# Optimization experiments

Hardware: AMD Instinct MI355X
Metric: run time of the kernel (lower is better)

## Reference

```python
import jax, jax.numpy as jnp
import numpy as np

B, S, F, D = 4, 1024, 8, 512
H = 8
DK = D // H
DF = 2048
ECLIPSE_BOOST = 2.0
LN_EPS = 1e-5


def _layer_norm(x, g, b):
    m = jnp.mean(x, axis=-1, keepdims=True)
    v = jnp.mean(jnp.square(x - m), axis=-1, keepdims=True)
    return (x - m) * jax.lax.rsqrt(v + LN_EPS) * g + b


def setup_inputs() -> dict:
    key = jax.random.key(0)
    ks = jax.random.split(key, 16)
    def lin_w(k, out_d, in_d):
        return jax.random.normal(k, (out_d, in_d), jnp.float32) * (1.0 / np.sqrt(in_d))
    return {
        "x": jax.random.normal(ks[0], (B, S, F, D), jnp.float32),
        "eclipse_mask": jax.random.bernoulli(ks[1], 0.3, (B, S)),
        "wq": lin_w(ks[2], D, D), "bq": jnp.zeros((D,), jnp.float32),
        "wk": lin_w(ks[3], D, D), "bk": jnp.zeros((D,), jnp.float32),
        "wv": lin_w(ks[4], D, D), "bv": jnp.zeros((D,), jnp.float32),
        "wo": lin_w(ks[5], D, D), "bo": jnp.zeros((D,), jnp.float32),
        "w1": lin_w(ks[6], DF, D), "b1": jnp.zeros((DF,), jnp.float32),
        "w2": lin_w(ks[7], D, DF), "b2": jnp.zeros((D,), jnp.float32),
        "g1": jnp.ones((D,), jnp.float32), "be1": jnp.zeros((D,), jnp.float32),
        "g2": jnp.ones((D,), jnp.float32), "be2": jnp.zeros((D,), jnp.float32),
    }


def reference(x, eclipse_mask, wq, bq, wk, bk, wv, bv, wo, bo, w1, b1, w2, b2, g1, be1, g2, be2):
    BF = B * F
    scale = 1.0 / np.sqrt(DK)
    # NOTE: the torch module does x.view(B*F, S, D) on a [B,S,F,D] tensor —
    # a raw memory reshape (NOT a transpose). Replicate exactly.
    xr = x.reshape(BF, S, D)  # [BF, S, D]
    # eclipse_mask [B,S] -> expand over features -> [BF, S] (rows b*F+f share mask[b])
    em = jnp.broadcast_to(eclipse_mask[:, None, :], (B, F, S)).reshape(BF, S)

    def proj(w, b):
        return (xr @ w.T + b).reshape(BF, S, H, DK).transpose(0, 2, 1, 3)  # [BF,H,S,DK]

    Q, K, V = proj(wq, bq), proj(wk, bk), proj(wv, bv)
    scores = jnp.einsum("bhqd,bhkd->bhqk", Q, K) * scale  # [BF,H,S,S]
    boost = jnp.where(em, ECLIPSE_BOOST, 1.0)[:, None, None, :]  # over key positions
    scores = scores * boost
    attn = jax.nn.softmax(scores, axis=-1)
    ctx = jnp.einsum("bhqk,bhkd->bhqd", attn, V)  # [BF,H,S,DK]
    ctx = ctx.transpose(0, 2, 1, 3).reshape(BF, S, D)
    attn_out = (ctx @ wo.T + bo).reshape(B, S, F, D)  # raw reshape back, matches torch

    h = _layer_norm(x + attn_out, g1, be1)
    ff = jax.nn.gelu(h @ w1.T + b1, approximate=False) @ w2.T + b2
    return _layer_norm(h + ff, g2, be2)
```

## Files before the change

kernel.cpp:

```cpp
#include <hip/hip_runtime.h>
#include <math.h>

typedef _Float16 half8 __attribute__((ext_vector_type(8)));
typedef float f32x4 __attribute__((ext_vector_type(4)));
typedef unsigned int u32;

#define AS1 __attribute__((address_space(1)))
#define AS3 __attribute__((address_space(3)))

__device__ __forceinline__ void g2lds16(const void* g, void* l) {
    __builtin_amdgcn_global_load_lds((const AS1 u32*)g, (AS3 u32*)l, 16, 0, 0);
}

__global__ __launch_bounds__(256)
void cvt_all(const float* __restrict__ x, const float* __restrict__ wq,
             const float* __restrict__ wk, const float* __restrict__ wv,
             const float* __restrict__ wo, const float* __restrict__ w1,
             const float* __restrict__ w2, _Float16* __restrict__ xh,
             _Float16* __restrict__ qkvw, _Float16* __restrict__ woh,
             _Float16* __restrict__ w1h, _Float16* __restrict__ w2h)
{
    const int bid = blockIdx.x;
    const float* src; _Float16* dst; int g;
    if (bid < 8192)      { src = x;  dst = xh;            g = bid*256 + threadIdx.x; }
    else if (bid < 8320) { src = wq; dst = qkvw;          g = (bid-8192)*256 + threadIdx.x; }
    else if (bid < 8448) { src = wk; dst = qkvw + 262144; g = (bid-8320)*256 + threadIdx.x; }
    else if (bid < 8576) { src = wv; dst = qkvw + 524288; g = (bid-8448)*256 + threadIdx.x; }
    else if (bid < 8704) { src = wo; dst = woh;           g = (bid-8576)*256 + threadIdx.x; }
    else if (bid < 9216) { src = w1; dst = w1h;           g = (bid-8704)*256 + threadIdx.x; }
    else                 { src = w2; dst = w2h;           g = (bid-9216)*256 + threadIdx.x; }
    const float4* p = (const float4*)src + (size_t)g * 2;
    float4 a = p[0], b = p[1];
    half8 h;
    h[0]=(_Float16)a.x; h[1]=(_Float16)a.y; h[2]=(_Float16)a.z; h[3]=(_Float16)a.w;
    h[4]=(_Float16)b.x; h[5]=(_Float16)b.y; h[6]=(_Float16)b.z; h[7]=(_Float16)b.w;
    *((half8*)dst + g) = h;
}

__global__ __launch_bounds__(256)
void pack_bias(const float* __restrict__ bq, const float* __restrict__ bk,
               const float* __restrict__ bv, float* __restrict__ o)
{
    const int i = blockIdx.x * 256 + threadIdx.x;
    o[i] = i < 512 ? bq[i] : (i < 1024 ? bk[i-512] : bv[i-1024]);
}

template<int MODE>
__global__ __launch_bounds__(256)
void gemm_bt(const _Float16* __restrict__ A, const _Float16* __restrict__ B,
             const float* __restrict__ bias, const float* __restrict__ resf,
             const _Float16* __restrict__ resh, void* __restrict__ Cout,
             int M, int N, int K)
{
    __shared__ __align__(16) _Float16 As[128 * 32];
    __shared__ __align__(16) _Float16 Bs[128 * 32];
    const int tid = threadIdx.x;
    const int lane = tid & 63;
    const int w = tid >> 6;
    const int wm = w >> 1, wn = w & 1;
    const int m0 = blockIdx.y * 128, n0 = blockIdx.x * 128;
    const int lrow = lane & 15;
    const int lk = (lane >> 4) * 8;

    f32x4 acc[4][4];
#pragma unroll
    for (int i = 0; i < 4; ++i)
#pragma unroll
        for (int j = 0; j < 4; ++j) acc[i][j] = (f32x4)0.0f;

    for (int k0 = 0; k0 < K; k0 += 32) {
#pragma unroll
        for (int i = 0; i < 2; ++i) {
            int gbase = i * 256 + w * 64;
            int g = gbase + lane;
            g2lds16(A + (size_t)(m0 + (g >> 2)) * K + k0 + (g & 3) * 8,
                    (char*)As + (size_t)gbase * 16);
            g2lds16(B + (size_t)(n0 + (g >> 2)) * K + k0 + (g & 3) * 8,
                    (char*)Bs + (size_t)gbase * 16);
        }
        __syncthreads();
        half8 af[4], bfr[4];
#pragma unroll
        for (int t = 0; t < 4; ++t) {
            af[t]  = *(const half8*)(As + (wm * 64 + t * 16 + lrow) * 32 + lk);
            bfr[t] = *(const half8*)(Bs + (wn * 64 + t * 16 + lrow) * 32 + lk);
        }
#pragma unroll
        for (int mi = 0; mi < 4; ++mi)
#pragma unroll
            for (int ni = 0; ni < 4; ++ni)
                acc[mi][ni] = __builtin_amdgcn_mfma_f32_16x16x32_f16(af[mi], bfr[ni], acc[mi][ni], 0, 0, 0);
        __syncthreads();
    }

    const int rq = (lane >> 4) * 4;
#pragma unroll
    for (int mi = 0; mi < 4; ++mi) {
#pragma unroll
        for (int ni = 0; ni < 4; ++ni) {
            const int col = n0 + wn * 64 + ni * 16 + lrow;
            const float bv = bias[col];
#pragma unroll
            for (int r = 0; r < 4; ++r) {
                const int row = m0 + wm * 64 + mi * 16 + rq + r;
                const size_t idx = (size_t)row * N + col;
                float v = acc[mi][ni][r] + bv;
                if (MODE == 0) {
                    ((_Float16*)Cout)[idx] = (_Float16)v;
                } else if (MODE == 1) {
                    float t2 = -1.5957691216057308f * v * fmaf(v * v, 0.044715f, 1.0f);
                    float e = __expf(t2);
                    ((_Float16*)Cout)[idx] = (_Float16)(v * __builtin_amdgcn_rcpf(1.0f + e));
                } else if (MODE == 2) {
                    ((float*)Cout)[idx] = v + resf[idx];
                } else {
                    ((float*)Cout)[idx] = v + (float)resh[idx];
                }
            }
        }
    }
}

__global__ __launch_bounds__(256)
void attn_fwd(const _Float16* __restrict__ QKV, const int* __restrict__ mask,
              _Float16* __restrict__ ctx)
{
    constexpr int SQ = 72;
    __shared__ __align__(16) _Float16 Ks[64 * SQ];
    __shared__ __align__(16) _Float16 Vts[64 * SQ];
    __shared__ __align__(16) _Float16 Ps[4][32 * SQ];
    __shared__ float scs[1024];

    const int tid = threadIdx.x;
    const int lane = tid & 63;
    const int w = tid >> 6;
    const int bf = blockIdx.y >> 3;
    const int hh = blockIdx.y & 7;
    const int q0 = blockIdx.x * 128;
    const int lrow = lane & 15;
    const int lq = lane >> 4;

    {
        const int* mrow = mask + (bf >> 3) * 1024;
        const int i = tid * 4;
        int4 mm = *(const int4*)(mrow + i);
        scs[i + 0] = mm.x ? 0.25f : 0.125f;
        scs[i + 1] = mm.y ? 0.25f : 0.125f;
        scs[i + 2] = mm.z ? 0.25f : 0.125f;
        scs[i + 3] = mm.w ? 0.25f : 0.125f;
    }

    half8 qf[2][2];
#pragma unroll
    for (int qi = 0; qi < 2; ++qi) {
        const _Float16* qp = QKV + (size_t)(bf * 1024 + q0 + w * 32 + qi * 16 + lrow) * 1536 + hh * 64 + lq * 8;
        qf[qi][0] = *(const half8*)qp;
        qf[qi][1] = *(const half8*)(qp + 32);
    }

    const _Float16* Kbase = QKV + (size_t)bf * 1024 * 1536 + 512 + hh * 64;
    const _Float16* Vbase = Kbase + 512;

    f32x4 acc[2][4];
#pragma unroll
    for (int qi = 0; qi < 2; ++qi)
#pragma unroll
        for (int d = 0; d < 4; ++d) acc[qi][d] = (f32x4)0.0f;
    float lpart[2][4] = {{0.f,0.f,0.f,0.f},{0.f,0.f,0.f,0.f}};
    _Float16* Pw = &Ps[w][0];

    for (int kt = 0; kt < 1024; kt += 64) {
        __syncthreads();
        {
            const int r = tid >> 3, c = (tid & 7) * 8;
            *(uint4*)&Ks[r * SQ + c]        = *(const uint4*)(Kbase + (size_t)(kt + r) * 1536 + c);
            *(uint4*)&Ks[(r + 32) * SQ + c] = *(const uint4*)(Kbase + (size_t)(kt + r + 32) * 1536 + c);
            const int key = lane, dvb = w * 16;
            const _Float16* vp = Vbase + (size_t)(kt + key) * 1536 + dvb;
            half8 v0 = *(const half8*)vp;
            half8 v1 = *(const half8*)(vp + 8);
#pragma unroll
            for (int j = 0; j < 8; ++j) Vts[(dvb + j) * SQ + key] = v0[j];
#pragma unroll
            for (int j = 0; j < 8; ++j) Vts[(dvb + 8 + j) * SQ + key] = v1[j];
        }
        __syncthreads();

#pragma unroll
        for (int nt = 0; nt < 4; ++nt) {
            half8 kf0 = *(const half8*)(Ks + (nt * 16 + lrow) * SQ + lq * 8);
            half8 kf1 = *(const half8*)(Ks + (nt * 16 + lrow) * SQ + 32 + lq * 8);
            const float sc = scs[kt + nt * 16 + lrow];
#pragma unroll
            for (int qi = 0; qi < 2; ++qi) {
                f32x4 s = (f32x4)0.0f;
                s = __builtin_amdgcn_mfma_f32_16x16x32_f16(qf[qi][0], kf0, s, 0, 0, 0);
                s = __builtin_amdgcn_mfma_f32_16x16x32_f16(qf[qi][1], kf1, s, 0, 0, 0);
#pragma unroll
                for (int r = 0; r < 4; ++r) {
                    float p = __expf(fmaf(s[r], sc, -5.0f));
                    lpart[qi][r] += p;
                    Pw[(qi * 16 + lq * 4 + r) * SQ + nt * 16 + lrow] = (_Float16)p;
                }
            }
        }

        half8 pf[2][2];
#pragma unroll
        for (int qi = 0; qi < 2; ++qi) {
            pf[qi][0] = *(const half8*)(Pw + (qi * 16 + lrow) * SQ + lq * 8);
            pf[qi][1] = *(const half8*)(Pw + (qi * 16 + lrow) * SQ + 32 + lq * 8);
        }
#pragma unroll
        for (int d = 0; d < 4; ++d) {
            half8 vf0 = *(const half8*)(Vts + (d * 16 + lrow) * SQ + lq * 8);
            half8 vf1 = *(const half8*)(Vts + (d * 16 + lrow) * SQ + 32 + lq * 8);
#pragma unroll
            for (int qi = 0; qi < 2; ++qi) {
                acc[qi][d] = __builtin_amdgcn_mfma_f32_16x16x32_f16(pf[qi][0], vf0, acc[qi][d], 0, 0, 0);
                acc[qi][d] = __builtin_amdgcn_mfma_f32_16x16x32_f16(pf[qi][1], vf1, acc[qi][d], 0, 0, 0);
            }
        }
    }

#pragma unroll
    for (int qi = 0; qi < 2; ++qi) {
#pragma unroll
        for (int r = 0; r < 4; ++r) {
            float l = lpart[qi][r];
            l += __shfl_xor(l, 1); l += __shfl_xor(l, 2);
            l += __shfl_xor(l, 4); l += __shfl_xor(l, 8);
            const float inv = 1.0f / l;
            const int row = q0 + w * 32 + qi * 16 + lq * 4 + r;
            _Float16* cp = ctx + ((size_t)bf * 1024 + row) * 512 + hh * 64;
#pragma unroll
            for (int d = 0; d < 4; ++d)
                cp[d * 16 + lrow] = (_Float16)(acc[qi][d][r] * inv);
        }
    }
}

template<int OUTH>
__global__ __launch_bounds__(256)
void ln_fused(const float* __restrict__ X, const float* __restrict__ gma,
              const float* __restrict__ bta, float* __restrict__ outF,
              _Float16* __restrict__ outH)
{
    const int row = blockIdx.x * 4 + (threadIdx.x >> 6);
    const int lane = threadIdx.x & 63;
    const float4* xr = (const float4*)(X + (size_t)row * 512);
    float4 a = xr[lane * 2], c = xr[lane * 2 + 1];
    float s  = a.x + a.y + a.z + a.w + c.x + c.y + c.z + c.w;
    float s2 = a.x * a.x + a.y * a.y + a.z * a.z + a.w * a.w
             + c.x * c.x + c.y * c.y + c.z * c.z + c.w * c.w;
#pragma unroll
    for (int m = 1; m < 64; m <<= 1) { s += __shfl_xor(s, m); s2 += __shfl_xor(s2, m); }
    const float mean = s * (1.0f / 512.0f);
    const float inv = rsqrtf(s2 * (1.0f / 512.0f) - mean * mean + 1e-5f);
    const float4* gp = (const float4*)gma;
    const float4* bp = (const float4*)bta;
    float4 g0 = gp[lane * 2], g1 = gp[lane * 2 + 1];
    float4 b0 = bp[lane * 2], b1 = bp[lane * 2 + 1];
    float4 o0, o1;
    o0.x = (a.x - mean) * inv * g0.x + b0.x; o0.y = (a.y - mean) * inv * g0.y + b0.y;
    o0.z = (a.z - mean) * inv * g0.z + b0.z; o0.w = (a.w - mean) * inv * g0.w + b0.w;
    o1.x = (c.x - mean) * inv * g1.x + b1.x; o1.y = (c.y - mean) * inv * g1.y + b1.y;
    o1.z = (c.z - mean) * inv * g1.z + b1.z; o1.w = (c.w - mean) * inv * g1.w + b1.w;
    if (OUTH) {
        half8 hv;
        hv[0] = (_Float16)o0.x; hv[1] = (_Float16)o0.y; hv[2] = (_Float16)o0.z; hv[3] = (_Float16)o0.w;
        hv[4] = (_Float16)o1.x; hv[5] = (_Float16)o1.y; hv[6] = (_Float16)o1.z; hv[7] = (_Float16)o1.w;
        *((half8*)(outH + (size_t)row * 512) + lane) = hv;
    } else {
        float4* op = (float4*)(outF + (size_t)row * 512);
        op[lane * 2] = o0; op[lane * 2 + 1] = o1;
    }
}

extern "C" void kernel_launch(void* const* d_in, const int* in_sizes, int n_in,
                              void* d_out, int out_size, void* d_ws, size_t ws_size,
                              hipStream_t stream)
{
    const float* x   = (const float*)d_in[0];
    const int* mask  = (const int*)d_in[1];
    const float* wq  = (const float*)d_in[2];  const float* bq  = (const float*)d_in[3];
    const float* wk  = (const float*)d_in[4];  const float* bk  = (const float*)d_in[5];
    const float* wv  = (const float*)d_in[6];  const float* bv  = (const float*)d_in[7];
    const float* wo  = (const float*)d_in[8];  const float* bo  = (const float*)d_in[9];
    const float* w1  = (const float*)d_in[10]; const float* b1  = (const float*)d_in[11];
    const float* w2  = (const float*)d_in[12]; const float* b2  = (const float*)d_in[13];
    const float* g1  = (const float*)d_in[14]; const float* be1 = (const float*)d_in[15];
    const float* g2  = (const float*)d_in[16]; const float* be2 = (const float*)d_in[17];
    float* out = (float*)d_out;

    char* ws = (char*)d_ws;
    _Float16* qkvh = (_Float16*)(ws);
    _Float16* ctxh = (_Float16*)(ws + 100663296);
    _Float16* gh   = (_Float16*)(ws);
    _Float16* xh   = (_Float16*)(ws + 134217728);
    float*    res  = (float*)   (ws + 134217728);
    _Float16* hhb  = (_Float16*)(ws + 201326592);
    float*    biasf= (float*)   (ws + 201326592);
    _Float16* qkvw = (_Float16*)(ws + 234881024);
    _Float16* woh  = (_Float16*)(ws + 236453888);
    _Float16* w1h  = (_Float16*)(ws + 236978176);
    _Float16* w2h  = (_Float16*)(ws + 239075328);

    dim3 blk(256);

    cvt_all<<<9728, blk, 0, stream>>>(x, wq, wk, wv, wo, w1, w2, xh, qkvw, woh, w1h, w2h);
    pack_bias<<<6, blk, 0, stream>>>(bq, bk, bv, biasf);

    gemm_bt<0><<<dim3(12, 256), blk, 0, stream>>>(xh, qkvw, biasf, nullptr, nullptr, qkvh, 32768, 1536, 512);

    attn_fwd<<<dim3(8, 256), blk, 0, stream>>>(qkvh, mask, ctxh);

    gemm_bt<2><<<dim3(4, 256), blk, 0, stream>>>(ctxh, woh, bo, x, nullptr, res, 32768, 512, 512);

    ln_fused<1><<<8192, blk, 0, stream>>>(res, g1, be1, nullptr, hhb);

    gemm_bt<1><<<dim3(16, 256), blk, 0, stream>>>(hhb, w1h, b1, nullptr, nullptr, gh, 32768, 2048, 512);

    gemm_bt<3><<<dim3(4, 256), blk, 0, stream>>>(gh, w2h, b2, nullptr, hhb, res, 32768, 512, 2048);

    ln_fused<0><<<8192, blk, 0, stream>>>(res, g2, be2, out, nullptr);
}
```

Measured before the change: 696.5 us.

## Store residual sums in fp16, double K-step in GEMM, read mask directly

The residual-plus-projection outputs feeding both layer norms are now stored as fp16 instead of fp32, which halves that intermediate traffic, and the layer-norm kernel reads half8 inputs. The GEMM now loads two 32-wide K slices per barrier pair, halving the number of syncs per K. Attention drops the shared-memory scale table and reads the mask from global memory inside the inner loop. Rounding the residual sum to fp16 before layer norm adds precision loss.

```diff
diff --git a/kernel.cpp b/kernel.cpp
--- a/kernel.cpp
+++ b/kernel.cpp
@@ -52,8 +52,8 @@
              const _Float16* __restrict__ resh, void* __restrict__ Cout,
              int M, int N, int K)
 {
-    __shared__ __align__(16) _Float16 As[128 * 32];
-    __shared__ __align__(16) _Float16 Bs[128 * 32];
+    __shared__ __align__(16) _Float16 As[2][128 * 32];
+    __shared__ __align__(16) _Float16 Bs[2][128 * 32];
     const int tid = threadIdx.x;
     const int lane = tid & 63;
     const int w = tid >> 6;
@@ -68,28 +68,34 @@
 #pragma unroll
         for (int j = 0; j < 4; ++j) acc[i][j] = (f32x4)0.0f;
 
-    for (int k0 = 0; k0 < K; k0 += 32) {
-#pragma unroll
-        for (int i = 0; i < 2; ++i) {
-            int gbase = i * 256 + w * 64;
-            int g = gbase + lane;
-            g2lds16(A + (size_t)(m0 + (g >> 2)) * K + k0 + (g & 3) * 8,
-                    (char*)As + (size_t)gbase * 16);
-            g2lds16(B + (size_t)(n0 + (g >> 2)) * K + k0 + (g & 3) * 8,
-                    (char*)Bs + (size_t)gbase * 16);
+    for (int k0 = 0; k0 < K; k0 += 64) {
+#pragma unroll
+        for (int p = 0; p < 2; ++p) {
+#pragma unroll
+            for (int i = 0; i < 2; ++i) {
+                int gbase = i * 256 + w * 64;
+                int g = gbase + lane;
+                g2lds16(A + (size_t)(m0 + (g >> 2)) * K + k0 + p * 32 + (g & 3) * 8,
+                        (char*)As[p] + (size_t)gbase * 16);
+                g2lds16(B + (size_t)(n0 + (g >> 2)) * K + k0 + p * 32 + (g & 3) * 8,
+                        (char*)Bs[p] + (size_t)gbase * 16);
+            }
         }
         __syncthreads();
-        half8 af[4], bfr[4];
-#pragma unroll
-        for (int t = 0; t < 4; ++t) {
-            af[t]  = *(const half8*)(As + (wm * 64 + t * 16 + lrow) * 32 + lk);
-            bfr[t] = *(const half8*)(Bs + (wn * 64 + t * 16 + lrow) * 32 + lk);
-        }
-#pragma unroll
-        for (int mi = 0; mi < 4; ++mi)
-#pragma unroll
-            for (int ni = 0; ni < 4; ++ni)
-                acc[mi][ni] = __builtin_amdgcn_mfma_f32_16x16x32_f16(af[mi], bfr[ni], acc[mi][ni], 0, 0, 0);
+#pragma unroll
+        for (int p = 0; p < 2; ++p) {
+            half8 af[4], bfr[4];
+#pragma unroll
+            for (int t = 0; t < 4; ++t) {
+                af[t]  = *(const half8*)(&As[p][0] + (wm * 64 + t * 16 + lrow) * 32 + lk);
+                bfr[t] = *(const half8*)(&Bs[p][0] + (wn * 64 + t * 16 + lrow) * 32 + lk);
+            }
+#pragma unroll
+            for (int mi = 0; mi < 4; ++mi)
+#pragma unroll
+                for (int ni = 0; ni < 4; ++ni)
+                    acc[mi][ni] = __builtin_amdgcn_mfma_f32_16x16x32_f16(af[mi], bfr[ni], acc[mi][ni], 0, 0, 0);
+        }
         __syncthreads();
     }
 
@@ -112,9 +118,9 @@
                     float e = __expf(t2);
                     ((_Float16*)Cout)[idx] = (_Float16)(v * __builtin_amdgcn_rcpf(1.0f + e));
                 } else if (MODE == 2) {
-                    ((float*)Cout)[idx] = v + resf[idx];
+                    ((_Float16*)Cout)[idx] = (_Float16)(v + resf[idx]);
                 } else {
-                    ((float*)Cout)[idx] = v + (float)resh[idx];
+                    ((_Float16*)Cout)[idx] = (_Float16)(v + (float)resh[idx]);
                 }
             }
         }
@@ -129,7 +135,6 @@
     __shared__ __align__(16) _Float16 Ks[64 * SQ];
     __shared__ __align__(16) _Float16 Vts[64 * SQ];
     __shared__ __align__(16) _Float16 Ps[4][32 * SQ];
-    __shared__ float scs[1024];
 
     const int tid = threadIdx.x;
     const int lane = tid & 63;
@@ -140,15 +145,7 @@
     const int lrow = lane & 15;
     const int lq = lane >> 4;
 
-    {
-        const int* mrow = mask + (bf >> 3) * 1024;
-        const int i = tid * 4;
-        int4 mm = *(const int4*)(mrow + i);
-        scs[i + 0] = mm.x ? 0.25f : 0.125f;
-        scs[i + 1] = mm.y ? 0.25f : 0.125f;
-        scs[i + 2] = mm.z ? 0.25f : 0.125f;
-        scs[i + 3] = mm.w ? 0.25f : 0.125f;
-    }
+    const int* mrow = mask + (bf >> 3) * 1024;
 
     half8 qf[2][2];
 #pragma unroll
@@ -190,7 +187,7 @@
         for (int nt = 0; nt < 4; ++nt) {
             half8 kf0 = *(const half8*)(Ks + (nt * 16 + lrow) * SQ + lq * 8);
             half8 kf1 = *(const half8*)(Ks + (nt * 16 + lrow) * SQ + 32 + lq * 8);
-            const float sc = scs[kt + nt * 16 + lrow];
+            const float sc = mrow[kt + nt * 16 + lrow] ? 0.25f : 0.125f;
 #pragma unroll
             for (int qi = 0; qi < 2; ++qi) {
                 f32x4 s = (f32x4)0.0f;
@@ -242,17 +239,19 @@
 
 template<int OUTH>
 __global__ __launch_bounds__(256)
-void ln_fused(const float* __restrict__ X, const float* __restrict__ gma,
+void ln_fused(const _Float16* __restrict__ X, const float* __restrict__ gma,
               const float* __restrict__ bta, float* __restrict__ outF,
               _Float16* __restrict__ outH)
 {
     const int row = blockIdx.x * 4 + (threadIdx.x >> 6);
     const int lane = threadIdx.x & 63;
-    const float4* xr = (const float4*)(X + (size_t)row * 512);
-    float4 a = xr[lane * 2], c = xr[lane * 2 + 1];
-    float s  = a.x + a.y + a.z + a.w + c.x + c.y + c.z + c.w;
-    float s2 = a.x * a.x + a.y * a.y + a.z * a.z + a.w * a.w
-             + c.x * c.x + c.y * c.y + c.z * c.z + c.w * c.w;
+    const half8 hv = *((const half8*)(X + (size_t)row * 512) + lane);
+    float v[8];
+#pragma unroll
+    for (int j = 0; j < 8; ++j) v[j] = (float)hv[j];
+    float s = 0.f, s2 = 0.f;
+#pragma unroll
+    for (int j = 0; j < 8; ++j) { s += v[j]; s2 = fmaf(v[j], v[j], s2); }
 #pragma unroll
     for (int m = 1; m < 64; m <<= 1) { s += __shfl_xor(s, m); s2 += __shfl_xor(s2, m); }
     const float mean = s * (1.0f / 512.0f);
@@ -261,19 +260,20 @@
     const float4* bp = (const float4*)bta;
     float4 g0 = gp[lane * 2], g1 = gp[lane * 2 + 1];
     float4 b0 = bp[lane * 2], b1 = bp[lane * 2 + 1];
-    float4 o0, o1;
-    o0.x = (a.x - mean) * inv * g0.x + b0.x; o0.y = (a.y - mean) * inv * g0.y + b0.y;
-    o0.z = (a.z - mean) * inv * g0.z + b0.z; o0.w = (a.w - mean) * inv * g0.w + b0.w;
-    o1.x = (c.x - mean) * inv * g1.x + b1.x; o1.y = (c.y - mean) * inv * g1.y + b1.y;
-    o1.z = (c.z - mean) * inv * g1.z + b1.z; o1.w = (c.w - mean) * inv * g1.w + b1.w;
+    float o[8];
+    o[0] = (v[0]-mean)*inv*g0.x + b0.x; o[1] = (v[1]-mean)*inv*g0.y + b0.y;
+    o[2] = (v[2]-mean)*inv*g0.z + b0.z; o[3] = (v[3]-mean)*inv*g0.w + b0.w;
+    o[4] = (v[4]-mean)*inv*g1.x + b1.x; o[5] = (v[5]-mean)*inv*g1.y + b1.y;
+    o[6] = (v[6]-mean)*inv*g1.z + b1.z; o[7] = (v[7]-mean)*inv*g1.w + b1.w;
     if (OUTH) {
-        half8 hv;
-        hv[0] = (_Float16)o0.x; hv[1] = (_Float16)o0.y; hv[2] = (_Float16)o0.z; hv[3] = (_Float16)o0.w;
-        hv[4] = (_Float16)o1.x; hv[5] = (_Float16)o1.y; hv[6] = (_Float16)o1.z; hv[7] = (_Float16)o1.w;
-        *((half8*)(outH + (size_t)row * 512) + lane) = hv;
+        half8 ho;
+#pragma unroll
+        for (int j = 0; j < 8; ++j) ho[j] = (_Float16)o[j];
+        *((half8*)(outH + (size_t)row * 512) + lane) = ho;
     } else {
         float4* op = (float4*)(outF + (size_t)row * 512);
-        op[lane * 2] = o0; op[lane * 2 + 1] = o1;
+        op[lane * 2]     = make_float4(o[0], o[1], o[2], o[3]);
+        op[lane * 2 + 1] = make_float4(o[4], o[5], o[6], o[7]);
     }
 }
 
@@ -294,17 +294,17 @@
     float* out = (float*)d_out;
 
     char* ws = (char*)d_ws;
-    _Float16* qkvh = (_Float16*)(ws);
-    _Float16* ctxh = (_Float16*)(ws + 100663296);
-    _Float16* gh   = (_Float16*)(ws);
-    _Float16* xh   = (_Float16*)(ws + 134217728);
-    float*    res  = (float*)   (ws + 134217728);
-    _Float16* hhb  = (_Float16*)(ws + 201326592);
-    float*    biasf= (float*)   (ws + 201326592);
-    _Float16* qkvw = (_Float16*)(ws + 234881024);
-    _Float16* woh  = (_Float16*)(ws + 236453888);
-    _Float16* w1h  = (_Float16*)(ws + 236978176);
-    _Float16* w2h  = (_Float16*)(ws + 239075328);
+    _Float16* qkvh  = (_Float16*)(ws);
+    _Float16* gh    = (_Float16*)(ws);
+    _Float16* ctxh  = (_Float16*)(ws + 100663296);
+    _Float16* xh    = (_Float16*)(ws + 134217728);
+    _Float16* resh16= (_Float16*)(ws + 134217728);
+    _Float16* hhb   = (_Float16*)(ws + 201326592);
+    float*    biasf = (float*)   (ws + 201326592);
+    _Float16* qkvw  = (_Float16*)(ws + 234881024);
+    _Float16* woh   = (_Float16*)(ws + 236453888);
+    _Float16* w1h   = (_Float16*)(ws + 236978176);
+    _Float16* w2h   = (_Float16*)(ws + 239075328);
 
     dim3 blk(256);
 
@@ -315,13 +315,13 @@
 
     attn_fwd<<<dim3(8, 256), blk, 0, stream>>>(qkvh, mask, ctxh);
 
-    gemm_bt<2><<<dim3(4, 256), blk, 0, stream>>>(ctxh, woh, bo, x, nullptr, res, 32768, 512, 512);
-
-    ln_fused<1><<<8192, blk, 0, stream>>>(res, g1, be1, nullptr, hhb);
+    gemm_bt<2><<<dim3(4, 256), blk, 0, stream>>>(ctxh, woh, bo, x, nullptr, resh16, 32768, 512, 512);
+
+    ln_fused<1><<<8192, blk, 0, stream>>>(resh16, g1, be1, nullptr, hhb);
 
     gemm_bt<1><<<dim3(16, 256), blk, 0, stream>>>(hhb, w1h, b1, nullptr, nullptr, gh, 32768, 2048, 512);
 
-    gemm_bt<3><<<dim3(4, 256), blk, 0, stream>>>(gh, w2h, b2, nullptr, hhb, res, 32768, 512, 2048);
-
-    ln_fused<0><<<8192, blk, 0, stream>>>(res, g2, be2, out, nullptr);
-}
+    gemm_bt<3><<<dim3(4, 256), blk, 0, stream>>>(gh, w2h, b2, nullptr, hhb, resh16, 32768, 512, 2048);
+
+    ln_fused<0><<<8192, blk, 0, stream>>>(resh16, g2, be2, out, nullptr);
+}
```

Result: no change. 699.0 us (+0.3%).
